# Performance work log

Measured on AMD Instinct MI355X. Metric: run time of the kernel, lower is better.

## Reference

```python
import jax, jax.numpy as jnp
import numpy as np

POOL = 7; SR = 2; SCALE = 1.0 / 16
NUM_CLASSES = 21
NMS_THR = 0.5; MIN_SIZE = 1.0; TOPK = 100; SCORE_THR = 0.05
BBOX_CLIP = float(np.log(1000.0 / 16))


def roi_align(feat, rois):
    # feat: [C,H,W]; rois: [P,4] xyxy in image coords. torchvision aligned=True, sampling_ratio=2.
    C, H, W = feat.shape
    S = POOL * SR
    x0r = rois[:, 0] * SCALE - 0.5
    y0r = rois[:, 1] * SCALE - 0.5
    bw = (rois[:, 2] - rois[:, 0]) * SCALE / POOL
    bh = (rois[:, 3] - rois[:, 1]) * SCALE / POOL
    t = (jnp.arange(S, dtype=feat.dtype) + 0.5) / SR  # sample offsets in bin units
    ys = y0r[:, None] + bh[:, None] * t  # [P,S]
    xs = x0r[:, None] + bw[:, None] * t  # [P,S]
    vy = (ys >= -1.0) & (ys <= H)
    vx = (xs >= -1.0) & (xs <= W)
    y = jnp.clip(ys, 0.0, H - 1)
    x = jnp.clip(xs, 0.0, W - 1)
    yl = jnp.floor(y).astype(jnp.int32); xl = jnp.floor(x).astype(jnp.int32)
    yh = jnp.minimum(yl + 1, H - 1);     xh = jnp.minimum(xl + 1, W - 1)
    ly = y - yl; lx = x - xl
    hy = 1.0 - ly; hx = 1.0 - lx

    def g(Yi, Xi):  # -> [C,P,S,S]
        return feat[:, Yi[:, :, None], Xi[:, None, :]]

    val = (g(yl, xl) * (hy[:, :, None] * hx[:, None, :])
         + g(yl, xh) * (hy[:, :, None] * lx[:, None, :])
         + g(yh, xl) * (ly[:, :, None] * hx[:, None, :])
         + g(yh, xh) * (ly[:, :, None] * lx[:, None, :]))
    val = val * (vy[:, :, None] & vx[:, None, :])[None].astype(feat.dtype)
    P = rois.shape[0]
    val = val.reshape(C, P, POOL, SR, POOL, SR).mean(axis=(3, 5))  # avg over 2x2 samples/bin
    return val.transpose(1, 0, 2, 3)  # [P,C,POOL,POOL]


def decode(pred, proposals):
    # pred: [N,K,4] (dx,dy,dw,dh); proposals: [N,4]
    w = proposals[:, 2] - proposals[:, 0]
    h = proposals[:, 3] - proposals[:, 1]
    cx = proposals[:, 0] + 0.5 * w
    cy = proposals[:, 1] + 0.5 * h
    dx, dy = pred[..., 0], pred[..., 1]
    dw = jnp.minimum(pred[..., 2], BBOX_CLIP)
    dh = jnp.minimum(pred[..., 3], BBOX_CLIP)
    pcx = dx * w[:, None] + cx[:, None]
    pcy = dy * h[:, None] + cy[:, None]
    pw = jnp.exp(dw) * w[:, None]
    ph = jnp.exp(dh) * h[:, None]
    return jnp.stack([pcx - 0.5 * pw, pcy - 0.5 * ph, pcx + 0.5 * pw, pcy + 0.5 * ph], axis=-1)


def box_iou(b):
    x1, y1, x2, y2 = b[:, 0], b[:, 1], b[:, 2], b[:, 3]
    area = (x2 - x1) * (y2 - y1)
    iw = jnp.maximum(jnp.minimum(x2[:, None], x2[None, :]) - jnp.maximum(x1[:, None], x1[None, :]), 0.0)
    ih = jnp.maximum(jnp.minimum(y2[:, None], y2[None, :]) - jnp.maximum(y1[:, None], y1[None, :]), 0.0)
    inter = iw * ih
    return inter / (area[:, None] + area[None, :] - inter)


def filter_predictions(boxes, labels, scores):
    # score threshold + min-size + per-class greedy NMS + topK, static shapes (padded to TOPK)
    N = scores.shape[0]
    ws = boxes[:, 2] - boxes[:, 0]
    hs = boxes[:, 3] - boxes[:, 1]
    valid = (scores > SCORE_THR) & (ws >= MIN_SIZE) & (hs >= MIN_SIZE)
    skey = jnp.where(valid, scores, -jnp.inf)
    order = jnp.argsort(-skey)
    b = boxes[order]; s = skey[order]; l = labels[order]; v = valid[order]
    # batched_nms via per-class coordinate offset
    off = jax.lax.stop_gradient(jnp.max(boxes) + 1.0)
    ob = jax.lax.stop_gradient(b) + (l.astype(b.dtype) * off)[:, None]
    iou = box_iou(ob)  # [N,N]
    idx = jnp.arange(N)

    def body(keep, i):
        sup = (iou[i] > NMS_THR) & keep[i] & (idx > i)
        return keep & ~sup, None

    keep, _ = jax.lax.scan(body, v, idx)
    rank = jnp.cumsum(keep) - 1
    final = keep & (rank < TOPK)
    pick = jnp.argsort(jnp.where(final, idx, N))[:TOPK]  # kept indices in score order, padded
    ok = final[pick]
    out_boxes = jnp.where(ok[:, None], b[pick], 0.0)
    out_scores = jnp.where(ok, s[pick], 0.0)
    out_labels = jnp.where(ok, l[pick], -1)
    return out_boxes, out_labels, out_scores


def roi_head_forward(image, feat, proposals, fc6_w, fc6_b, fc7_w, fc7_b, cls_w, cls_b, reg_w, reg_b):
    H_img, W_img = image.shape[-2], image.shape[-1]
    pooled = roi_align(feat[0], proposals)  # [P,C,7,7]
    x = pooled.reshape(pooled.shape[0], -1)
    x = jax.nn.relu(x @ fc6_w.T + fc6_b)
    x = jax.nn.relu(x @ fc7_w.T + fc7_b)
    cls_scores = x @ cls_w.T + cls_b                       # [P,K]
    box_pred = (x @ reg_w.T + reg_b).reshape(-1, NUM_CLASSES, 4)
    boxes = decode(box_pred, proposals)                    # [P,K,4]
    scores = jax.nn.softmax(cls_scores, axis=-1)
    boxes = jnp.stack([boxes[..., 0].clip(0, W_img), boxes[..., 1].clip(0, H_img),
                       boxes[..., 2].clip(0, W_img), boxes[..., 3].clip(0, H_img)], axis=-1)
    labels = jnp.broadcast_to(jnp.arange(NUM_CLASSES), scores.shape)
    boxes = boxes[:, 1:].reshape(-1, 4)
    scores = scores[:, 1:].reshape(-1)
    labels = (labels[:, 1:] - 1).reshape(-1)
    return filter_predictions(boxes, labels, scores)


def setup_inputs() -> dict:
    key = jax.random.key(0)
    ks = jax.random.split(key, 12)
    H_img, W_img = 800, 1072
    P, C = 300, 512
    image = jnp.zeros((1, 3, H_img, W_img), jnp.float32)
    feat = jax.random.normal(ks[0], (1, C, H_img // 16, W_img // 16), jnp.float32)
    cx = jax.random.uniform(ks[1], (P,)) * W_img
    cy = jax.random.uniform(ks[2], (P,)) * H_img
    bw = 20.0 + jax.random.uniform(ks[3], (P,)) * 300.0
    bh = 20.0 + jax.random.uniform(ks[4], (P,)) * 300.0
    proposals = jnp.stack([jnp.clip(cx - bw / 2, 0, W_img), jnp.clip(cy - bh / 2, 0, H_img),
                           jnp.clip(cx + bw / 2, 0, W_img), jnp.clip(cy + bh / 2, 0, H_img)], axis=1)
    fin = C * POOL * POOL  # 25088
    D = 1024
    fc6_w = jax.random.normal(ks[5], (D, fin), jnp.float32) / np.sqrt(fin)
    fc6_b = jnp.zeros((D,), jnp.float32)
    fc7_w = jax.random.normal(ks[6], (D, D), jnp.float32) / np.sqrt(D)
    fc7_b = jnp.zeros((D,), jnp.float32)
    cls_w = jax.random.normal(ks[7], (NUM_CLASSES, D), jnp.float32) / np.sqrt(D)
    cls_b = jnp.zeros((NUM_CLASSES,), jnp.float32)
    reg_w = jax.random.normal(ks[8], (NUM_CLASSES * 4, D), jnp.float32) * 0.001
    reg_b = jnp.zeros((NUM_CLASSES * 4,), jnp.float32)
    return {"image": image, "feat": feat, "proposals": proposals,
            "fc6_w": fc6_w, "fc6_b": fc6_b, "fc7_w": fc7_w, "fc7_b": fc7_b,
            "cls_w": cls_w, "cls_b": cls_b, "reg_w": reg_w, "reg_b": reg_b}


def reference(image, feat, proposals, fc6_w, fc6_b, fc7_w, fc7_b, cls_w, cls_b, reg_w, reg_b):
    return roi_head_forward(image, feat, proposals, fc6_w, fc6_b, fc7_w, fc7_b, cls_w, cls_b, reg_w, reg_b)
```

## Files before the change

kernel.cpp:

```cpp
#include <hip/hip_runtime.h>
#include <hip/hip_bf16.h>
#include <math.h>

#define P_N   300
#define C_N   512
#define H_F   50
#define W_F   67
#define HW_F  3350
#define D_N   1024
#define FIN   25088
#define NCLS  21
#define NCAND 6000
#define W_IMG 1072.0f
#define H_IMG 800.0f
#define BBOX_CLIP_F 4.135166556742356f
#define KS6   28
#define STEPS6_PER_Z 28
#define KS7   16
#define STEPS7_PER_Z 2
#define KSH   16
#define STEPSH_PER_Z 2
#define NHEAD 128
#define NW    96
#define A_SCALE 16.0f
#define B_SCALE 256.0f
#define O_SCALE (1.0f / 4096.0f)
#define TBLK  1680

typedef __attribute__((ext_vector_type(8)))  _Float16 half8;
typedef __attribute__((ext_vector_type(16))) float    f32x16;

__device__ __forceinline__ void splitA(float f, _Float16& h, _Float16& l) {
  float fs = f * A_SCALE;
  h = (_Float16)fs;
  l = (_Float16)(fs - (float)h);
}

__device__ __forceinline__ int swz(int slot, int ks) {
  return slot ^ ((slot >> 5) & 1) ^ (((slot >> 3) & 1) << 1) ^ ((ks & 1) << 2);
}

__device__ __forceinline__ int blob_half_idx(int row, int j8) {
  const int ksW = j8 >> 1, kc8 = j8 & 1;
  const int mf = row >> 5;
  return (mf * 2 + ksW) * 512 + swz((kc8 << 5) | (row & 31), ksW) * 8;
}

__global__ __launch_bounds__(256) void prep_transpose(const float* __restrict__ feat,
                                                      float* __restrict__ ft,
                                                      const float* __restrict__ cls_w,
                                                      const float* __restrict__ cls_b,
                                                      const float* __restrict__ reg_w,
                                                      const float* __restrict__ reg_b,
                                                      float* __restrict__ Wpad,
                                                      float* __restrict__ bpad,
                                                      int* __restrict__ vcount) {
  __shared__ float tile[32][33];
  const int bid = blockIdx.x;
  const int tid = threadIdx.x;
  if (bid < TBLK) {
    const int bx = bid % 105, byy = bid / 105;
    const int s0 = bx * 32, c0 = byy * 32;
    const int tx = tid & 31, ty = tid >> 5;
    for (int r = ty; r < 32; r += 8) {
      int c = c0 + r, s = s0 + tx;
      tile[r][tx] = (s < HW_F) ? feat[(size_t)c * HW_F + s] : 0.0f;
    }
    __syncthreads();
    for (int r = ty; r < 32; r += 8) {
      int s = s0 + r, c = c0 + tx;
      if (s < HW_F) ft[(size_t)s * C_N + c] = tile[tx][r];
    }
  } else {
    const int row = bid - TBLK;
    if (row == 0 && tid == 0) *vcount = 0;
    const float* src = (row < NCLS) ? (cls_w + (size_t)row * D_N)
                     : (row < 105)  ? (reg_w + (size_t)(row - NCLS) * D_N) : nullptr;
    float4 v = make_float4(0.f, 0.f, 0.f, 0.f);
    if (src) v = reinterpret_cast<const float4*>(src)[tid];
    reinterpret_cast<float4*>(Wpad + (size_t)row * D_N)[tid] = v;
    if (tid == 0)
      bpad[row] = (row < NCLS) ? cls_b[row] : (row < 105) ? reg_b[row - NCLS] : 0.0f;
  }
}

__global__ __launch_bounds__(256, 3) void roi_align_k(const float* __restrict__ ft,
                                                      const float* __restrict__ rois,
                                                      _Float16* __restrict__ Xhi,
                                                      _Float16* __restrict__ Xlo) {
  __shared__ _Float16 hbuf[12544] __attribute__((aligned(16)));
  __shared__ _Float16 lbuf[12544] __attribute__((aligned(16)));
  __shared__ float g_ly[14], g_hy[14], g_lx[14], g_hx[14];
  __shared__ int   g_yoL[14], g_yoH[14], g_xoL[14], g_xoH[14];

  const int p   = blockIdx.x;
  const int ch  = blockIdx.y;
  const int tid = threadIdx.x;

  if (tid < 14) {
    const float rx0 = rois[p*4+0], ry0 = rois[p*4+1], rx1 = rois[p*4+2], ry1 = rois[p*4+3];
    const float x0r = rx0 * 0.0625f - 0.5f;
    const float y0r = ry0 * 0.0625f - 0.5f;
    const float bw  = (rx1 - rx0) * 0.0625f * (1.0f / 7.0f);
    const float bh  = (ry1 - ry0) * 0.0625f * (1.0f / 7.0f);
    const float t   = ((float)tid + 0.5f) * 0.5f;

    const float ys = y0r + bh * t;
    const bool vy = (ys >= -1.0f) && (ys <= (float)H_F);
    float y = fminf(fmaxf(ys, 0.0f), (float)(H_F - 1));
    int yi = (int)floorf(y);
    const int yh = min(yi + 1, H_F - 1);
    float ly = y - (float)yi, hy = 1.0f - (y - (float)yi);
    if (!vy) { ly = 0.0f; hy = 0.0f; }
    g_ly[tid] = ly; g_hy[tid] = hy;
    g_yoL[tid] = yi * (W_F * C_N); g_yoH[tid] = yh * (W_F * C_N);

    const float xs = x0r + bw * t;
    const bool vx = (xs >= -1.0f) && (xs <= (float)W_F);
    float x = fminf(fmaxf(xs, 0.0f), (float)(W_F - 1));
    int xi = (int)floorf(x);
    const int xh = min(xi + 1, W_F - 1);
    float lx = x - (float)xi, hx = 1.0f - (x - (float)xi);
    if (!vx) { lx = 0.0f; hx = 0.0f; }
    g_lx[tid] = lx; g_hx[tid] = hx;
    g_xoL[tid] = xi * C_N; g_xoH[tid] = xh * C_N;
  }
  __syncthreads();

  const float* ftc = ft + ch * 256 + tid;
#pragma unroll 4
  for (int cell = 0; cell < 49; ++cell) {
    const int py = cell / 7;
    const int px = cell - py * 7;
    float acc = 0.0f;
#pragma unroll
    for (int sy = 0; sy < 2; ++sy) {
      const int iy = 2 * py + sy;
      const float ly = g_ly[iy], hy = g_hy[iy];
      const int yoL = g_yoL[iy], yoH = g_yoH[iy];
#pragma unroll
      for (int sx = 0; sx < 2; ++sx) {
        const int ix = 2 * px + sx;
        const float lx = g_lx[ix], hx = g_hx[ix];
        const int xoL = g_xoL[ix], xoH = g_xoH[ix];
        acc += (hy*hx)*ftc[yoL+xoL] + (hy*lx)*ftc[yoL+xoH]
             + (ly*hx)*ftc[yoH+xoL] + (ly*lx)*ftc[yoH+xoH];
      }
    }
    _Float16 h, l;
    splitA(acc * 0.25f, h, l);
    hbuf[tid * 49 + cell] = h;
    lbuf[tid * 49 + cell] = l;
  }
  __syncthreads();

  const size_t base = (size_t)p * FIN + (size_t)ch * 12544;
  const uint4* hs = (const uint4*)hbuf;
  const uint4* ls = (const uint4*)lbuf;
  uint4* dh = (uint4*)(Xhi + base);
  uint4* dl = (uint4*)(Xlo + base);
  for (int k = tid; k < 1568; k += 256) { dh[k] = hs[k]; dl[k] = ls[k]; }
}

__global__ __launch_bounds__(256) void reshuffle_x(const _Float16* __restrict__ Shi,
                                                   const _Float16* __restrict__ Slo,
                                                   char* __restrict__ blob,
                                                   int M2, int K) {
  __shared__ _Float16 buf[8192] __attribute__((aligned(16)));
  const int tile = blockIdx.x, step = blockIdx.y;
  const int tid = threadIdx.x;
  const int steps = K >> 5;
#pragma unroll
  for (int i = 0; i < 4; ++i) {
    const int g = tid + i * 256;
    const int half = g >> 9;
    const int row = (g >> 2) & 127;
    const int j8 = g & 3;
    const int gm = tile * 128 + row;
    uint4 v = make_uint4(0, 0, 0, 0);
    if (gm < M2) {
      const _Float16* src = (half ? Slo : Shi) + (size_t)gm * K + (step << 5) + (j8 << 3);
      v = *reinterpret_cast<const uint4*>(src);
    }
    *reinterpret_cast<uint4*>(buf + half * 4096 + blob_half_idx(row, j8)) = v;
  }
  __syncthreads();
  uint4* dst = (uint4*)(blob + (((size_t)tile * steps + step) << 14));
  const uint4* s = (const uint4*)buf;
#pragma unroll
  for (int i = 0; i < 4; ++i) dst[tid + i * 256] = s[tid + i * 256];
}

__global__ __launch_bounds__(256, 3) void gemm_f16_3p(
    const char* __restrict__ Ablob, const float* __restrict__ Wt, float* __restrict__ Pt,
    int M, int K, int steps_per_z, int ldc)
{
  __shared__ _Float16 lds[16384] __attribute__((aligned(16)));
  const int tid  = threadIdx.x;
  const int lane = tid & 63, wave = tid >> 6;
  const int wm = wave >> 1, wn = wave & 1;

  const int GX = gridDim.x, GY = gridDim.y;
  const int T  = GX * GY * gridDim.z;
  int flat = blockIdx.x + GX * (blockIdx.y + GY * blockIdx.z);
  if ((T & 7) == 0) flat = (flat & 7) * (T >> 3) + (flat >> 3);
  const int bx = flat % GX;
  const int by = (flat / GX) % GY;
  const int bz = flat / (GX * GY);

  const int m0 = bx * 128, n0 = by * 128;
  const int steps_total = K >> 5;
  const int s0 = bz * steps_per_z;
  const int s1 = min(s0 + steps_per_z, steps_total);

  f32x16 acc[2][2];
#pragma unroll
  for (int a = 0; a < 2; ++a)
#pragma unroll
    for (int b = 0; b < 2; ++b)
#pragma unroll
      for (int r = 0; r < 16; ++r) acc[a][b][r] = 0.f;

  const int srow = tid >> 2;
  const int j8   = tid & 3;
  const int ksW  = j8 >> 1, kc8 = j8 & 1;
  const int wslot = swz((kc8 << 5) | (srow & 31), ksW);

  for (int step = s0; step < s1; ++step) {
    const int kb = step << 5;
    const char* Ab = Ablob + (((size_t)bx * steps_total + step) << 14);
#pragma unroll
    for (int c2 = 0; c2 < 4; ++c2) {
      const int off = ((wave << 2) + c2) << 10;
      __builtin_amdgcn_global_load_lds(
          (const __attribute__((address_space(1))) uint32_t*)(Ab + off + (lane << 4)),
          (__attribute__((address_space(3))) uint32_t*)((char*)lds + off),
          16, 0, 0);
    }
#pragma unroll
    for (int half = 0; half < 2; ++half) {
      const int n = srow + half * 64;
      const float* wp = Wt + (size_t)(n0 + n) * K + kb + j8 * 8;
      const float4 f0 = *reinterpret_cast<const float4*>(wp);
      const float4 f1 = *reinterpret_cast<const float4*>(wp + 4);
      float fv[8] = {f0.x, f0.y, f0.z, f0.w, f1.x, f1.y, f1.z, f1.w};
      union { _Float16 h[8]; uint4 v; } uh, ul;
#pragma unroll
      for (int e = 0; e < 8; ++e) {
        float fs = fv[e] * B_SCALE;
        uh.h[e] = (_Float16)fs;
        ul.h[e] = (_Float16)(fs - (float)uh.h[e]);
      }
      const int nf = n >> 5;
      const int base = 8192 + (nf * 2 + ksW) * 512 + wslot * 8;
      *reinterpret_cast<uint4*>(&lds[base])        = uh.v;
      *reinterpret_cast<uint4*>(&lds[4096 + base]) = ul.v;
    }
    __syncthreads();
#pragma unroll
    for (int ks = 0; ks < 2; ++ks) {
      const int rslot = swz(lane, ks) * 8;
      half8 ah[2], al[2], bh[2], bl[2];
#pragma unroll
      for (int mi = 0; mi < 2; ++mi) {
        const int mf = wm * 2 + mi;
        ah[mi] = *reinterpret_cast<const half8*>(&lds[(mf * 2 + ks) * 512 + rslot]);
        al[mi] = *reinterpret_cast<const half8*>(&lds[4096 + (mf * 2 + ks) * 512 + rslot]);
      }
#pragma unroll
      for (int ni = 0; ni < 2; ++ni) {
        const int nf = wn * 2 + ni;
        bh[ni] = *reinterpret_cast<const half8*>(&lds[8192  + (nf * 2 + ks) * 512 + rslot]);
        bl[ni] = *reinterpret_cast<const half8*>(&lds[12288 + (nf * 2 + ks) * 512 + rslot]);
      }
#pragma unroll
      for (int mi = 0; mi < 2; ++mi)
#pragma unroll
        for (int ni = 0; ni < 2; ++ni) {
          acc[mi][ni] = __builtin_amdgcn_mfma_f32_32x32x16_f16(ah[mi], bh[ni], acc[mi][ni], 0, 0, 0);
          acc[mi][ni] = __builtin_amdgcn_mfma_f32_32x32x16_f16(ah[mi], bl[ni], acc[mi][ni], 0, 0, 0);
          acc[mi][ni] = __builtin_amdgcn_mfma_f32_32x32x16_f16(al[mi], bh[ni], acc[mi][ni], 0, 0, 0);
        }
    }
    __syncthreads();
  }
  const int col = lane & 31, rhi = lane >> 5;
  float* outp = Pt + (size_t)bz * ((size_t)M * ldc);
#pragma unroll
  for (int mi = 0; mi < 2; ++mi)
#pragma unroll
    for (int ni = 0; ni < 2; ++ni) {
      const int n = n0 + (wn * 2 + ni) * 32 + col;
      if (n >= ldc) continue;
#pragma unroll
      for (int r = 0; r < 16; ++r) {
        const int m = m0 + (wm * 2 + mi) * 32 + ((r & 3) + 8 * (r >> 2) + 4 * rhi);
        if (m < M) outp[(size_t)m * ldc + n] = acc[mi][ni][r] * O_SCALE;
      }
    }
}

__global__ __launch_bounds__(256) void reduce_frag(const float* __restrict__ Pt,
                                                   const float* __restrict__ bias,
                                                   char* __restrict__ blob,
                                                   int KS, int stepsB) {
  const int g = blockIdx.x * 256 + threadIdx.x;
  if (g >= P_N * 128) return;
  const int m = g >> 7;
  const int gg = g & 127;
  const int n0 = gg << 3;
  float s[8];
#pragma unroll
  for (int e = 0; e < 8; ++e) s[e] = bias[n0 + e];
  for (int k2 = 0; k2 < KS; ++k2) {
    const float* pp = Pt + ((size_t)k2 * P_N + m) * D_N + n0;
    const float4 a = *reinterpret_cast<const float4*>(pp);
    const float4 b = *reinterpret_cast<const float4*>(pp + 4);
    s[0]+=a.x; s[1]+=a.y; s[2]+=a.z; s[3]+=a.w;
    s[4]+=b.x; s[5]+=b.y; s[6]+=b.z; s[7]+=b.w;
  }
  union { _Float16 h[8]; uint4 v; } uh, ul;
#pragma unroll
  for (int e = 0; e < 8; ++e) {
    float r = fmaxf(s[e], 0.0f);
    _Float16 h, l; splitA(r, h, l);
    uh.h[e] = h; ul.h[e] = l;
  }
  const int tile = m >> 7, row = m & 127;
  const int step = gg >> 2, j8 = gg & 3;
  _Float16* dst = (_Float16*)(blob + (((size_t)tile * stepsB + step) << 14));
  const int hidx = blob_half_idx(row, j8);
  *reinterpret_cast<uint4*>(dst + hidx) = uh.v;
  *reinterpret_cast<uint4*>(dst + 4096 + hidx) = ul.v;
}

__global__ __launch_bounds__(256) void reduce_bias(const float* __restrict__ Pt,
                                                   const float* __restrict__ bias,
                                                   float* __restrict__ out_f32,
                                                   int MN, int KS, int nmask) {
  int i = blockIdx.x * 256 + threadIdx.x;
  if (i >= MN) return;
  float s = 0.0f;
  for (int k = 0; k < KS; ++k) s += Pt[(size_t)k * MN + i];
  s += bias[i & nmask];
  out_f32[i] = s;
}

__global__ __launch_bounds__(64) void decode_kernel(const float* __restrict__ logits,
                                                    const float* __restrict__ props,
                                                    float* __restrict__ cboxes,
                                                    unsigned long long* __restrict__ ckeys,
                                                    int* __restrict__ vcount) {
  const int p = blockIdx.x;
  const int lane = threadIdx.x;
  const float* lg = logits + (size_t)p * NHEAD;

  float s = (lane < NCLS) ? lg[lane] : -__builtin_inff();
  float mx = s;
#pragma unroll
  for (int off = 32; off > 0; off >>= 1) mx = fmaxf(mx, __shfl_xor(mx, off));
  float e = (lane < NCLS) ? expf(s - mx) : 0.0f;
  float sum = e;
#pragma unroll
  for (int off = 32; off > 0; off >>= 1) sum += __shfl_xor(sum, off);
  const float sm = e / sum;

  if (lane >= 1 && lane < NCLS) {
    const int c = lane;
    const float x0 = props[p*4+0], y0 = props[p*4+1], x1 = props[p*4+2], y1 = props[p*4+3];
    const float w = x1 - x0, hh = y1 - y0;
    const float cx = x0 + 0.5f * w, cy = y0 + 0.5f * hh;
    const float dx = lg[NCLS + c*4 + 0];
    const float dy = lg[NCLS + c*4 + 1];
    const float dw = fminf(lg[NCLS + c*4 + 2], BBOX_CLIP_F);
    const float dh = fminf(lg[NCLS + c*4 + 3], BBOX_CLIP_F);
    const float pcx = dx * w + cx, pcy = dy * hh + cy;
    const float pw = expf(dw) * w, ph = expf(dh) * hh;
    float bx0 = pcx - 0.5f * pw, by0 = pcy - 0.5f * ph;
    float bx1 = pcx + 0.5f * pw, by1 = pcy + 0.5f * ph;
    bx0 = fminf(fmaxf(bx0, 0.0f), W_IMG);
    by0 = fminf(fmaxf(by0, 0.0f), H_IMG);
    bx1 = fminf(fmaxf(bx1, 0.0f), W_IMG);
    by1 = fminf(fmaxf(by1, 0.0f), H_IMG);
    const int idx = p * 20 + (c - 1);
    cboxes[idx*4+0] = bx0; cboxes[idx*4+1] = by0;
    cboxes[idx*4+2] = bx1; cboxes[idx*4+3] = by1;
    const bool valid = (sm > 0.05f) && ((bx1 - bx0) >= 1.0f) && ((by1 - by0) >= 1.0f);
    if (valid) {
      int pos = atomicAdd(vcount, 1);
      unsigned u = __float_as_uint(sm);
      ckeys[pos] = ((unsigned long long)(~u) << 32) | (unsigned)idx;
    }
  }
}

__global__ __launch_bounds__(1024) void sort_gather(const unsigned long long* __restrict__ ckeys,
                                                    const int* __restrict__ vcount,
                                                    const float* __restrict__ cboxes,
                                                    float4* __restrict__ sbox,
                                                    float* __restrict__ sscore,
                                                    int* __restrict__ slab) {
  __shared__ unsigned long long keys[8192];
  const int tid = threadIdx.x;
  const int V = *vcount;
  int Npad = 64; while (Npad < V) Npad <<= 1;
  for (int i = tid; i < Npad; i += 1024)
    keys[i] = (i < V) ? ckeys[i] : ~0ULL;
  __syncthreads();
  for (int kk = 2; kk <= Npad; kk <<= 1) {
    for (int j = kk >> 1; j > 0; j >>= 1) {
      for (int i = tid; i < Npad; i += 1024) {
        int ij = i ^ j;
        if (ij > i) {
          unsigned long long a = keys[i], b = keys[ij];
          bool up = ((i & kk) == 0);
          if ((a > b) == up) { keys[i] = b; keys[ij] = a; }
        }
      }
      __syncthreads();
    }
  }
  for (int i = tid; i < V; i += 1024) {
    unsigned long long key = keys[i];
    int idx = (int)(key & 0xffffffffu);
    sbox[i]   = *reinterpret_cast<const float4*>(&cboxes[(size_t)idx * 4]);
    sscore[i] = __uint_as_float(~(unsigned)(key >> 32));
    slab[i]   = idx % 20;
  }
}

__global__ __launch_bounds__(256) void iou_matrix(const float4* __restrict__ sbox,
                                                  const int* __restrict__ slab,
                                                  const int* __restrict__ vcount,
                                                  unsigned long long* __restrict__ mask) {
  const int V = *vcount;
  const int i = blockIdx.x * 4 + (threadIdx.x >> 6);
  const int lane = threadIdx.x & 63;
  if (i >= V) return;
  const float4 bi = sbox[i];
  const int li = slab[i];
  const float ai = (bi.z - bi.x) * (bi.w - bi.y);
  const int nw = (V + 63) >> 6;
  for (int w = 0; w < nw; ++w) {
    const int j = (w << 6) + lane;
    bool sup = false;
    if (j > i && j < V && slab[j] == li) {
      const float4 bj = sbox[j];
      const float iw = fminf(bi.z, bj.z) - fmaxf(bi.x, bj.x);
      const float ih = fminf(bi.w, bj.w) - fmaxf(bi.y, bj.y);
      const float inter = fmaxf(iw, 0.0f) * fmaxf(ih, 0.0f);
      const float aj = (bj.z - bj.x) * (bj.w - bj.y);
      sup = inter / (ai + aj - inter) > 0.5f;
    }
    const unsigned long long m = __ballot(sup);
    if (lane == 0) mask[(size_t)i * NW + w] = m;
  }
}

__device__ __forceinline__ unsigned long long bcast_live(unsigned long long live0,
                                                         unsigned long long live1, int w) {
  union { unsigned long long u; uint2 v; } t;
  t.u = (w < 64) ? live0 : live1;
  const int src = w & 63;
  const unsigned lo = __shfl(t.v.x, src);
  const unsigned hi = __shfl(t.v.y, src);
  return ((unsigned long long)hi << 32) | lo;
}

__global__ __launch_bounds__(64) void nms_scan(const float4* __restrict__ sbox,
                                               const float* __restrict__ sscore,
                                               const int* __restrict__ slab,
                                               const int* __restrict__ vcount,
                                               const unsigned long long* __restrict__ mask,
                                               float* __restrict__ out) {
  const int lane = threadIdx.x;
  const int V = min(*vcount, NCAND);
  const int nw = (V + 63) >> 6;
  unsigned long long live0 = ~0ULL, live1 = ~0ULL;
  int nk = 0;
  for (int w = 0; w < nw && nk < 100; ++w) {
    const int nb = V - (w << 6);
    const unsigned long long vmask = (nb >= 64) ? ~0ULL : ((1ULL << nb) - 1ULL);
    unsigned long long wv = bcast_live(live0, live1, w) & vmask;
    while (wv && nk < 100) {
      const int b = __ffsll((long long)wv) - 1;
      const int i = (w << 6) + b;
      if (lane == 0) {
        const float4 bb = sbox[i];
        out[nk*4+0] = bb.x; out[nk*4+1] = bb.y; out[nk*4+2] = bb.z; out[nk*4+3] = bb.w;
        out[400 + nk] = (float)slab[i];
        out[500 + nk] = sscore[i];
      }
      const unsigned long long* mrow = mask + (size_t)i * NW;
      if (lane < nw) live0 &= ~mrow[lane];
      if (64 + lane < nw) live1 &= ~mrow[64 + lane];
      nk++;
      wv = bcast_live(live0, live1, w) & vmask;
      wv &= (b == 63) ? 0ULL : ~((2ULL << b) - 1ULL);
    }
  }
  for (int r = nk + lane; r < 100; r += 64) {
    out[r*4+0] = 0.0f; out[r*4+1] = 0.0f; out[r*4+2] = 0.0f; out[r*4+3] = 0.0f;
    out[400 + r] = -1.0f;
    out[500 + r] = 0.0f;
  }
}

extern "C" void kernel_launch(void* const* d_in, const int* in_sizes, int n_in,
                              void* d_out, int out_size, void* d_ws, size_t ws_size,
                              hipStream_t stream) {
  const float* feat   = (const float*)d_in[1];
  const float* props  = (const float*)d_in[2];
  const float* fc6_w  = (const float*)d_in[3];
  const float* fc6_b  = (const float*)d_in[4];
  const float* fc7_w  = (const float*)d_in[5];
  const float* fc7_b  = (const float*)d_in[6];
  const float* cls_w  = (const float*)d_in[7];
  const float* cls_b  = (const float*)d_in[8];
  const float* reg_w  = (const float*)d_in[9];
  const float* reg_b  = (const float*)d_in[10];

  char* ws = (char*)d_ws;
  const size_t XSZ = (size_t)P_N * FIN * 2;
  const size_t R1  = (size_t)KS6 * P_N * D_N * 4;
  _Float16* Xhi = (_Float16*)ws;
  _Float16* Xlo = (_Float16*)(ws + XSZ);
  float*    Pt  = (float*)ws;
  char* reg2 = ws + R1;
  float* ft   = (float*)reg2;
  char*  Xb   = reg2;
  const size_t XBSZ = (size_t)3 * 784 * 16384;
  size_t off = R1 + XBSZ;
  auto alloc = [&](size_t bytes) -> void* {
    void* p = ws + off;
    off += (bytes + 255) & ~(size_t)255;
    return p;
  };
  char*  h6b   = (char*)alloc((size_t)3 * 32 * 16384);
  char*  h7b   = (char*)alloc((size_t)3 * 32 * 16384);
  float* Wpad  = (float*)alloc((size_t)NHEAD * D_N * 4);
  float* bpad  = (float*)alloc((size_t)NHEAD * 4);
  float* logits= (float*)alloc((size_t)P_N * NHEAD * 4);
  float* cboxes= (float*)alloc((size_t)NCAND * 4 * 4);
  unsigned long long* ckeys = (unsigned long long*)alloc((size_t)NCAND * 8);
  float4* sbox = (float4*)alloc((size_t)NCAND * 16);
  float* sscore= (float*)alloc((size_t)NCAND * 4);
  int*   slab  = (int*)alloc((size_t)NCAND * 4);
  unsigned long long* supmask = (unsigned long long*)alloc((size_t)NCAND * NW * 8);
  int*   vcount= (int*)alloc(256);
  (void)ws_size; (void)in_sizes; (void)n_in; (void)out_size;

  prep_transpose<<<TBLK + NHEAD, 256, 0, stream>>>(feat, ft, cls_w, cls_b, reg_w, reg_b,
                                                   Wpad, bpad, vcount);
  roi_align_k<<<dim3(P_N, 2), 256, 0, stream>>>(ft, props, Xhi, Xlo);
  reshuffle_x<<<dim3(3, 784), 256, 0, stream>>>(Xhi, Xlo, Xb, P_N, FIN);
  gemm_f16_3p<<<dim3(3, 8, KS6), 256, 0, stream>>>(Xb, fc6_w, Pt, P_N, FIN, STEPS6_PER_Z, D_N);
  reduce_frag<<<150, 256, 0, stream>>>(Pt, fc6_b, h6b, KS6, 32);
  gemm_f16_3p<<<dim3(3, 8, KS7), 256, 0, stream>>>(h6b, fc7_w, Pt, P_N, D_N, STEPS7_PER_Z, D_N);
  reduce_frag<<<150, 256, 0, stream>>>(Pt, fc7_b, h7b, KS7, 32);
  gemm_f16_3p<<<dim3(3, 1, KSH), 256, 0, stream>>>(h7b, Wpad, Pt, P_N, D_N, STEPSH_PER_Z, NHEAD);
  reduce_bias<<<(P_N * NHEAD + 255) / 256, 256, 0, stream>>>(
      Pt, bpad, logits, P_N * NHEAD, KSH, NHEAD - 1);
  decode_kernel<<<P_N, 64, 0, stream>>>(logits, props, cboxes, ckeys, vcount);
  sort_gather<<<1, 1024, 0, stream>>>(ckeys, vcount, cboxes, sbox, sscore, slab);
  iou_matrix<<<(NCAND + 3) / 4, 256, 0, stream>>>(sbox, slab, vcount, supmask);
  nms_scan<<<1, 64, 0, stream>>>(sbox, sscore, slab, vcount, supmask, (float*)d_out);
}
```

Before: 339.3 us.

## Double-buffer LDS in split-K GEMM and widen block to 512 threads

```diff
diff --git a/kernel.cpp b/kernel.cpp
--- a/kernel.cpp
+++ b/kernel.cpp
@@ -191,14 +191,14 @@
   for (int i = 0; i < 4; ++i) dst[tid + i * 256] = s[tid + i * 256];
 }
 
-__global__ __launch_bounds__(256, 3) void gemm_f16_3p(
+__global__ __launch_bounds__(512, 4) void gemm_f16_3p(
     const char* __restrict__ Ablob, const float* __restrict__ Wt, float* __restrict__ Pt,
     int M, int K, int steps_per_z, int ldc)
 {
-  __shared__ _Float16 lds[16384] __attribute__((aligned(16)));
+  __shared__ _Float16 lds[32768] __attribute__((aligned(16)));
   const int tid  = threadIdx.x;
   const int lane = tid & 63, wave = tid >> 6;
-  const int wm = wave >> 1, wn = wave & 1;
+  const int wm = wave >> 2, wn = wave & 3;
 
   const int GX = gridDim.x, GY = gridDim.y;
   const int T  = GX * GY * gridDim.z;
@@ -213,91 +213,92 @@
   const int s0 = bz * steps_per_z;
   const int s1 = min(s0 + steps_per_z, steps_total);
 
-  f32x16 acc[2][2];
+  f32x16 acc[2];
 #pragma unroll
   for (int a = 0; a < 2; ++a)
 #pragma unroll
-    for (int b = 0; b < 2; ++b)
-#pragma unroll
-      for (int r = 0; r < 16; ++r) acc[a][b][r] = 0.f;
+    for (int r = 0; r < 16; ++r) acc[a][r] = 0.f;
 
   const int srow = tid >> 2;
   const int j8   = tid & 3;
   const int ksW  = j8 >> 1, kc8 = j8 & 1;
   const int wslot = swz((kc8 << 5) | (srow & 31), ksW);
-
-  for (int step = s0; step < s1; ++step) {
+  const int nfB  = srow >> 5;
+
+  auto stage = [&](int buf, int step) {
     const int kb = step << 5;
+    char* ldsb = (char*)lds + (buf << 15);
     const char* Ab = Ablob + (((size_t)bx * steps_total + step) << 14);
 #pragma unroll
-    for (int c2 = 0; c2 < 4; ++c2) {
-      const int off = ((wave << 2) + c2) << 10;
+    for (int c2 = 0; c2 < 2; ++c2) {
+      const int off = ((wave * 2 + c2) << 10);
       __builtin_amdgcn_global_load_lds(
           (const __attribute__((address_space(1))) uint32_t*)(Ab + off + (lane << 4)),
-          (__attribute__((address_space(3))) uint32_t*)((char*)lds + off),
+          (__attribute__((address_space(3))) uint32_t*)(ldsb + off),
           16, 0, 0);
     }
-#pragma unroll
-    for (int half = 0; half < 2; ++half) {
-      const int n = srow + half * 64;
-      const float* wp = Wt + (size_t)(n0 + n) * K + kb + j8 * 8;
-      const float4 f0 = *reinterpret_cast<const float4*>(wp);
-      const float4 f1 = *reinterpret_cast<const float4*>(wp + 4);
-      float fv[8] = {f0.x, f0.y, f0.z, f0.w, f1.x, f1.y, f1.z, f1.w};
-      union { _Float16 h[8]; uint4 v; } uh, ul;
-#pragma unroll
-      for (int e = 0; e < 8; ++e) {
-        float fs = fv[e] * B_SCALE;
-        uh.h[e] = (_Float16)fs;
-        ul.h[e] = (_Float16)(fs - (float)uh.h[e]);
-      }
-      const int nf = n >> 5;
-      const int base = 8192 + (nf * 2 + ksW) * 512 + wslot * 8;
-      *reinterpret_cast<uint4*>(&lds[base])        = uh.v;
-      *reinterpret_cast<uint4*>(&lds[4096 + base]) = ul.v;
-    }
-    __syncthreads();
+    const float* wp = Wt + (size_t)(n0 + srow) * K + kb + j8 * 8;
+    const float4 f0 = *reinterpret_cast<const float4*>(wp);
+    const float4 f1 = *reinterpret_cast<const float4*>(wp + 4);
+    float fv[8] = {f0.x, f0.y, f0.z, f0.w, f1.x, f1.y, f1.z, f1.w};
+    union { _Float16 h[8]; uint4 v; } uh, ul;
+#pragma unroll
+    for (int e = 0; e < 8; ++e) {
+      float fs = fv[e] * B_SCALE;
+      uh.h[e] = (_Float16)fs;
+      ul.h[e] = (_Float16)(fs - (float)uh.h[e]);
+    }
+    _Float16* ldsh = (_Float16*)ldsb;
+    const int base = 8192 + (nfB * 2 + ksW) * 512 + wslot * 8;
+    *reinterpret_cast<uint4*>(&ldsh[base])        = uh.v;
+    *reinterpret_cast<uint4*>(&ldsh[4096 + base]) = ul.v;
+  };
+
+  auto compute = [&](int buf) {
+    _Float16* ldsh = (_Float16*)((char*)lds + (buf << 15));
 #pragma unroll
     for (int ks = 0; ks < 2; ++ks) {
       const int rslot = swz(lane, ks) * 8;
-      half8 ah[2], al[2], bh[2], bl[2];
+      half8 ah[2], al[2], bh, bl;
 #pragma unroll
       for (int mi = 0; mi < 2; ++mi) {
         const int mf = wm * 2 + mi;
-        ah[mi] = *reinterpret_cast<const half8*>(&lds[(mf * 2 + ks) * 512 + rslot]);
-        al[mi] = *reinterpret_cast<const half8*>(&lds[4096 + (mf * 2 + ks) * 512 + rslot]);
+        ah[mi] = *reinterpret_cast<const half8*>(&ldsh[(mf * 2 + ks) * 512 + rslot]);
+        al[mi] = *reinterpret_cast<const half8*>(&ldsh[4096 + (mf * 2 + ks) * 512 + rslot]);
       }
-#pragma unroll
-      for (int ni = 0; ni < 2; ++ni) {
-        const int nf = wn * 2 + ni;
-        bh[ni] = *reinterpret_cast<const half8*>(&lds[8192  + (nf * 2 + ks) * 512 + rslot]);
-        bl[ni] = *reinterpret_cast<const half8*>(&lds[12288 + (nf * 2 + ks) * 512 + rslot]);
+      bh = *reinterpret_cast<const half8*>(&ldsh[8192  + (wn * 2 + ks) * 512 + rslot]);
+      bl = *reinterpret_cast<const half8*>(&ldsh[12288 + (wn * 2 + ks) * 512 + rslot]);
+#pragma unroll
+      for (int mi = 0; mi < 2; ++mi) {
+        acc[mi] = __builtin_amdgcn_mfma_f32_32x32x16_f16(ah[mi], bh, acc[mi], 0, 0, 0);
+        acc[mi] = __builtin_amdgcn_mfma_f32_32x32x16_f16(ah[mi], bl, acc[mi], 0, 0, 0);
+        acc[mi] = __builtin_amdgcn_mfma_f32_32x32x16_f16(al[mi], bh, acc[mi], 0, 0, 0);
       }
-#pragma unroll
-      for (int mi = 0; mi < 2; ++mi)
-#pragma unroll
-        for (int ni = 0; ni < 2; ++ni) {
-          acc[mi][ni] = __builtin_amdgcn_mfma_f32_32x32x16_f16(ah[mi], bh[ni], acc[mi][ni], 0, 0, 0);
-          acc[mi][ni] = __builtin_amdgcn_mfma_f32_32x32x16_f16(ah[mi], bl[ni], acc[mi][ni], 0, 0, 0);
-          acc[mi][ni] = __builtin_amdgcn_mfma_f32_32x32x16_f16(al[mi], bh[ni], acc[mi][ni], 0, 0, 0);
-        }
-    }
+    }
+  };
+
+  if (s0 < s1) stage(0, s0);
+  __syncthreads();
+  int cur = 0;
+  for (int s = s0; s < s1; ++s) {
+    if (s + 1 < s1) stage(cur ^ 1, s + 1);
+    compute(cur);
     __syncthreads();
-  }
+    cur ^= 1;
+  }
+
   const int col = lane & 31, rhi = lane >> 5;
   float* outp = Pt + (size_t)bz * ((size_t)M * ldc);
-#pragma unroll
-  for (int mi = 0; mi < 2; ++mi)
-#pragma unroll
-    for (int ni = 0; ni < 2; ++ni) {
-      const int n = n0 + (wn * 2 + ni) * 32 + col;
-      if (n >= ldc) continue;
+  const int n = n0 + wn * 32 + col;
+  if (n < ldc) {
+#pragma unroll
+    for (int mi = 0; mi < 2; ++mi)
 #pragma unroll
       for (int r = 0; r < 16; ++r) {
         const int m = m0 + (wm * 2 + mi) * 32 + ((r & 3) + 8 * (r >> 2) + 4 * rhi);
-        if (m < M) outp[(size_t)m * ldc + n] = acc[mi][ni][r] * O_SCALE;
+        if (m < M) outp[(size_t)m * ldc + n] = acc[mi][r] * O_SCALE;
       }
-    }
+  }
 }
 
 __global__ __launch_bounds__(256) void reduce_frag(const float* __restrict__ Pt,
@@ -554,11 +555,11 @@
                                                    Wpad, bpad, vcount);
   roi_align_k<<<dim3(P_N, 2), 256, 0, stream>>>(ft, props, Xhi, Xlo);
   reshuffle_x<<<dim3(3, 784), 256, 0, stream>>>(Xhi, Xlo, Xb, P_N, FIN);
-  gemm_f16_3p<<<dim3(3, 8, KS6), 256, 0, stream>>>(Xb, fc6_w, Pt, P_N, FIN, STEPS6_PER_Z, D_N);
+  gemm_f16_3p<<<dim3(3, 8, KS6), 512, 0, stream>>>(Xb, fc6_w, Pt, P_N, FIN, STEPS6_PER_Z, D_N);
   reduce_frag<<<150, 256, 0, stream>>>(Pt, fc6_b, h6b, KS6, 32);
-  gemm_f16_3p<<<dim3(3, 8, KS7), 256, 0, stream>>>(h6b, fc7_w, Pt, P_N, D_N, STEPS7_PER_Z, D_N);
+  gemm_f16_3p<<<dim3(3, 8, KS7), 512, 0, stream>>>(h6b, fc7_w, Pt, P_N, D_N, STEPS7_PER_Z, D_N);
   reduce_frag<<<150, 256, 0, stream>>>(Pt, fc7_b, h7b, KS7, 32);
-  gemm_f16_3p<<<dim3(3, 1, KSH), 256, 0, stream>>>(h7b, Wpad, Pt, P_N, D_N, STEPSH_PER_Z, NHEAD);
+  gemm_f16_3p<<<dim3(3, 1, KSH), 512, 0, stream>>>(h7b, Wpad, Pt, P_N, D_N, STEPSH_PER_Z, NHEAD);
   reduce_bias<<<(P_N * NHEAD + 255) / 256, 256, 0, stream>>>(
       Pt, bpad, logits, P_N * NHEAD, KSH, NHEAD - 1);
   decode_kernel<<<P_N, 64, 0, stream>>>(logits, props, cboxes, ckeys, vcount);
```

Result: slower. 352.1 us (+3.8%).

## Double-buffer GEMM LDS tiles and fuse head split-K reduction into decode

Applied to the files above, without the earlier changes.

```diff
diff --git a/kernel.cpp b/kernel.cpp
--- a/kernel.cpp
+++ b/kernel.cpp
@@ -191,11 +191,11 @@
   for (int i = 0; i < 4; ++i) dst[tid + i * 256] = s[tid + i * 256];
 }
 
-__global__ __launch_bounds__(256, 3) void gemm_f16_3p(
+__global__ __launch_bounds__(256, 2) void gemm_f16_3p(
     const char* __restrict__ Ablob, const float* __restrict__ Wt, float* __restrict__ Pt,
     int M, int K, int steps_per_z, int ldc)
 {
-  __shared__ _Float16 lds[16384] __attribute__((aligned(16)));
+  __shared__ _Float16 lds[32768] __attribute__((aligned(16)));
   const int tid  = threadIdx.x;
   const int lane = tid & 63, wave = tid >> 6;
   const int wm = wave >> 1, wn = wave & 1;
@@ -225,65 +225,101 @@
   const int j8   = tid & 3;
   const int ksW  = j8 >> 1, kc8 = j8 & 1;
   const int wslot = swz((kc8 << 5) | (srow & 31), ksW);
-
-  for (int step = s0; step < s1; ++step) {
-    const int kb = step << 5;
+  const int nf0 = srow >> 5;
+  const int nf1 = (srow + 64) >> 5;
+
+  auto issueA = [&](int buf, int step) {
     const char* Ab = Ablob + (((size_t)bx * steps_total + step) << 14);
+    char* ldsb = (char*)lds + (buf << 15);
 #pragma unroll
     for (int c2 = 0; c2 < 4; ++c2) {
       const int off = ((wave << 2) + c2) << 10;
       __builtin_amdgcn_global_load_lds(
           (const __attribute__((address_space(1))) uint32_t*)(Ab + off + (lane << 4)),
-          (__attribute__((address_space(3))) uint32_t*)((char*)lds + off),
+          (__attribute__((address_space(3))) uint32_t*)(ldsb + off),
           16, 0, 0);
     }
-#pragma unroll
-    for (int half = 0; half < 2; ++half) {
-      const int n = srow + half * 64;
-      const float* wp = Wt + (size_t)(n0 + n) * K + kb + j8 * 8;
-      const float4 f0 = *reinterpret_cast<const float4*>(wp);
-      const float4 f1 = *reinterpret_cast<const float4*>(wp + 4);
-      float fv[8] = {f0.x, f0.y, f0.z, f0.w, f1.x, f1.y, f1.z, f1.w};
-      union { _Float16 h[8]; uint4 v; } uh, ul;
-#pragma unroll
-      for (int e = 0; e < 8; ++e) {
-        float fs = fv[e] * B_SCALE;
-        uh.h[e] = (_Float16)fs;
-        ul.h[e] = (_Float16)(fs - (float)uh.h[e]);
-      }
-      const int nf = n >> 5;
-      const int base = 8192 + (nf * 2 + ksW) * 512 + wslot * 8;
-      *reinterpret_cast<uint4*>(&lds[base])        = uh.v;
-      *reinterpret_cast<uint4*>(&lds[4096 + base]) = ul.v;
-    }
-    __syncthreads();
+  };
+  auto loadB = [&](int step, float4& g0, float4& g1, float4& g2, float4& g3) {
+    const int kb = step << 5;
+    const float* wp0 = Wt + (size_t)(n0 + srow) * K + kb + j8 * 8;
+    const float* wp1 = Wt + (size_t)(n0 + srow + 64) * K + kb + j8 * 8;
+    g0 = *reinterpret_cast<const float4*>(wp0);
+    g1 = *reinterpret_cast<const float4*>(wp0 + 4);
+    g2 = *reinterpret_cast<const float4*>(wp1);
+    g3 = *reinterpret_cast<const float4*>(wp1 + 4);
+  };
+  auto writeB = [&](int buf, float4 g0, float4 g1, float4 g2, float4 g3) {
+    _Float16* ldsh = (_Float16*)((char*)lds + (buf << 15));
+    float fv0[8] = {g0.x, g0.y, g0.z, g0.w, g1.x, g1.y, g1.z, g1.w};
+    float fv1[8] = {g2.x, g2.y, g2.z, g2.w, g3.x, g3.y, g3.z, g3.w};
+    union { _Float16 h[8]; uint4 v; } uh0, ul0, uh1, ul1;
+#pragma unroll
+    for (int e = 0; e < 8; ++e) {
+      float fs0 = fv0[e] * B_SCALE;
+      uh0.h[e] = (_Float16)fs0;
+      ul0.h[e] = (_Float16)(fs0 - (float)uh0.h[e]);
+      float fs1 = fv1[e] * B_SCALE;
+      uh1.h[e] = (_Float16)fs1;
+      ul1.h[e] = (_Float16)(fs1 - (float)uh1.h[e]);
+    }
+    const int base0 = 8192 + (nf0 * 2 + ksW) * 512 + wslot * 8;
+    const int base1 = 8192 + (nf1 * 2 + ksW) * 512 + wslot * 8;
+    *reinterpret_cast<uint4*>(&ldsh[base0])        = uh0.v;
+    *reinterpret_cast<uint4*>(&ldsh[4096 + base0]) = ul0.v;
+    *reinterpret_cast<uint4*>(&ldsh[base1])        = uh1.v;
+    *reinterpret_cast<uint4*>(&ldsh[4096 + base1]) = ul1.v;
+  };
+
+  if (s0 < s1) {
+    issueA(0, s0);
+    float4 g0, g1, g2, g3;
+    loadB(s0, g0, g1, g2, g3);
+    writeB(0, g0, g1, g2, g3);
+  }
+  __syncthreads();
+
+  int cur = 0;
+  for (int s = s0; s < s1; ++s) {
+    _Float16* ldsh = (_Float16*)((char*)lds + (cur << 15));
+    half8 ah[2][2], al[2][2], bh[2][2], bl[2][2];
 #pragma unroll
     for (int ks = 0; ks < 2; ++ks) {
       const int rslot = swz(lane, ks) * 8;
-      half8 ah[2], al[2], bh[2], bl[2];
 #pragma unroll
       for (int mi = 0; mi < 2; ++mi) {
         const int mf = wm * 2 + mi;
-        ah[mi] = *reinterpret_cast<const half8*>(&lds[(mf * 2 + ks) * 512 + rslot]);
-        al[mi] = *reinterpret_cast<const half8*>(&lds[4096 + (mf * 2 + ks) * 512 + rslot]);
+        ah[ks][mi] = *reinterpret_cast<const half8*>(&ldsh[(mf * 2 + ks) * 512 + rslot]);
+        al[ks][mi] = *reinterpret_cast<const half8*>(&ldsh[4096 + (mf * 2 + ks) * 512 + rslot]);
       }
 #pragma unroll
       for (int ni = 0; ni < 2; ++ni) {
         const int nf = wn * 2 + ni;
-        bh[ni] = *reinterpret_cast<const half8*>(&lds[8192  + (nf * 2 + ks) * 512 + rslot]);
-        bl[ni] = *reinterpret_cast<const half8*>(&lds[12288 + (nf * 2 + ks) * 512 + rslot]);
+        bh[ks][ni] = *reinterpret_cast<const half8*>(&ldsh[8192  + (nf * 2 + ks) * 512 + rslot]);
+        bl[ks][ni] = *reinterpret_cast<const half8*>(&ldsh[12288 + (nf * 2 + ks) * 512 + rslot]);
       }
+    }
+    const bool hasNext = (s + 1 < s1);
+    float4 g0, g1, g2, g3;
+    if (hasNext) {
+      issueA(cur ^ 1, s + 1);
+      loadB(s + 1, g0, g1, g2, g3);
+    }
+#pragma unroll
+    for (int ks = 0; ks < 2; ++ks)
 #pragma unroll
       for (int mi = 0; mi < 2; ++mi)
 #pragma unroll
         for (int ni = 0; ni < 2; ++ni) {
-          acc[mi][ni] = __builtin_amdgcn_mfma_f32_32x32x16_f16(ah[mi], bh[ni], acc[mi][ni], 0, 0, 0);
-          acc[mi][ni] = __builtin_amdgcn_mfma_f32_32x32x16_f16(ah[mi], bl[ni], acc[mi][ni], 0, 0, 0);
-          acc[mi][ni] = __builtin_amdgcn_mfma_f32_32x32x16_f16(al[mi], bh[ni], acc[mi][ni], 0, 0, 0);
+          acc[mi][ni] = __builtin_amdgcn_mfma_f32_32x32x16_f16(ah[ks][mi], bh[ks][ni], acc[mi][ni], 0, 0, 0);
+          acc[mi][ni] = __builtin_amdgcn_mfma_f32_32x32x16_f16(ah[ks][mi], bl[ks][ni], acc[mi][ni], 0, 0, 0);
+          acc[mi][ni] = __builtin_amdgcn_mfma_f32_32x32x16_f16(al[ks][mi], bh[ks][ni], acc[mi][ni], 0, 0, 0);
         }
-    }
+    if (hasNext) writeB(cur ^ 1, g0, g1, g2, g3);
     __syncthreads();
-  }
+    cur ^= 1;
+  }
+
   const int col = lane & 31, rhi = lane >> 5;
   float* outp = Pt + (size_t)bz * ((size_t)M * ldc);
 #pragma unroll
@@ -334,26 +370,23 @@
   *reinterpret_cast<uint4*>(dst + 4096 + hidx) = ul.v;
 }
 
-__global__ __launch_bounds__(256) void reduce_bias(const float* __restrict__ Pt,
-                                                   const float* __restrict__ bias,
-                                                   float* __restrict__ out_f32,
-                                                   int MN, int KS, int nmask) {
-  int i = blockIdx.x * 256 + threadIdx.x;
-  if (i >= MN) return;
-  float s = 0.0f;
-  for (int k = 0; k < KS; ++k) s += Pt[(size_t)k * MN + i];
-  s += bias[i & nmask];
-  out_f32[i] = s;
-}
-
-__global__ __launch_bounds__(64) void decode_kernel(const float* __restrict__ logits,
+__global__ __launch_bounds__(64) void decode_kernel(const float* __restrict__ Pt,
+                                                    const float* __restrict__ bpad,
                                                     const float* __restrict__ props,
                                                     float* __restrict__ cboxes,
                                                     unsigned long long* __restrict__ ckeys,
                                                     int* __restrict__ vcount) {
   const int p = blockIdx.x;
   const int lane = threadIdx.x;
-  const float* lg = logits + (size_t)p * NHEAD;
+  __shared__ float lg[NHEAD];
+
+  for (int o = lane; o < NHEAD; o += 64) {
+    float s = 0.0f;
+    for (int k = 0; k < KSH; ++k)
+      s += Pt[((size_t)k * P_N + p) * NHEAD + o];
+    lg[o] = s + bpad[o];
+  }
+  __syncthreads();
 
   float s = (lane < NCLS) ? lg[lane] : -__builtin_inff();
   float mx = s;
@@ -540,7 +573,6 @@
   char*  h7b   = (char*)alloc((size_t)3 * 32 * 16384);
   float* Wpad  = (float*)alloc((size_t)NHEAD * D_N * 4);
   float* bpad  = (float*)alloc((size_t)NHEAD * 4);
-  float* logits= (float*)alloc((size_t)P_N * NHEAD * 4);
   float* cboxes= (float*)alloc((size_t)NCAND * 4 * 4);
   unsigned long long* ckeys = (unsigned long long*)alloc((size_t)NCAND * 8);
   float4* sbox = (float4*)alloc((size_t)NCAND * 16);
@@ -559,9 +591,7 @@
   gemm_f16_3p<<<dim3(3, 8, KS7), 256, 0, stream>>>(h6b, fc7_w, Pt, P_N, D_N, STEPS7_PER_Z, D_N);
   reduce_frag<<<150, 256, 0, stream>>>(Pt, fc7_b, h7b, KS7, 32);
   gemm_f16_3p<<<dim3(3, 1, KSH), 256, 0, stream>>>(h7b, Wpad, Pt, P_N, D_N, STEPSH_PER_Z, NHEAD);
-  reduce_bias<<<(P_N * NHEAD + 255) / 256, 256, 0, stream>>>(
-      Pt, bpad, logits, P_N * NHEAD, KSH, NHEAD - 1);
-  decode_kernel<<<P_N, 64, 0, stream>>>(logits, props, cboxes, ckeys, vcount);
+  decode_kernel<<<P_N, 64, 0, stream>>>(Pt, bpad, props, cboxes, ckeys, vcount);
   sort_gather<<<1, 1024, 0, stream>>>(ckeys, vcount, cboxes, sbox, sscore, slab);
   iou_matrix<<<(NCAND + 3) / 4, 256, 0, stream>>>(sbox, slab, vcount, supmask);
   nms_scan<<<1, 64, 0, stream>>>(sbox, sscore, slab, vcount, supmask, (float*)d_out);
```

New measurement: 345.1 us. Within noise of the previous version (+1.7%).

## Process two K-steps per GEMM barrier and fuse head reduction into decode

Applied to the files above, without the earlier changes.

```diff
diff --git a/kernel.cpp b/kernel.cpp
--- a/kernel.cpp
+++ b/kernel.cpp
@@ -191,11 +191,11 @@
   for (int i = 0; i < 4; ++i) dst[tid + i * 256] = s[tid + i * 256];
 }
 
-__global__ __launch_bounds__(256, 3) void gemm_f16_3p(
+__global__ __launch_bounds__(256) void gemm_f16_3p(
     const char* __restrict__ Ablob, const float* __restrict__ Wt, float* __restrict__ Pt,
     int M, int K, int steps_per_z, int ldc)
 {
-  __shared__ _Float16 lds[16384] __attribute__((aligned(16)));
+  __shared__ _Float16 lds[32768] __attribute__((aligned(16)));
   const int tid  = threadIdx.x;
   const int lane = tid & 63, wave = tid >> 6;
   const int wm = wave >> 1, wn = wave & 1;
@@ -225,62 +225,72 @@
   const int j8   = tid & 3;
   const int ksW  = j8 >> 1, kc8 = j8 & 1;
   const int wslot = swz((kc8 << 5) | (srow & 31), ksW);
-
-  for (int step = s0; step < s1; ++step) {
-    const int kb = step << 5;
-    const char* Ab = Ablob + (((size_t)bx * steps_total + step) << 14);
-#pragma unroll
-    for (int c2 = 0; c2 < 4; ++c2) {
-      const int off = ((wave << 2) + c2) << 10;
+  const int nf0 = srow >> 5;
+  const int nf1 = (srow + 64) >> 5;
+
+  for (int s = s0; s < s1; s += 2) {
+    const char* Ab = Ablob + (((size_t)bx * steps_total + s) << 14);
+#pragma unroll
+    for (int c2 = 0; c2 < 8; ++c2) {
+      const int off = ((wave << 3) + c2) << 10;
       __builtin_amdgcn_global_load_lds(
           (const __attribute__((address_space(1))) uint32_t*)(Ab + off + (lane << 4)),
           (__attribute__((address_space(3))) uint32_t*)((char*)lds + off),
           16, 0, 0);
     }
 #pragma unroll
-    for (int half = 0; half < 2; ++half) {
-      const int n = srow + half * 64;
-      const float* wp = Wt + (size_t)(n0 + n) * K + kb + j8 * 8;
-      const float4 f0 = *reinterpret_cast<const float4*>(wp);
-      const float4 f1 = *reinterpret_cast<const float4*>(wp + 4);
-      float fv[8] = {f0.x, f0.y, f0.z, f0.w, f1.x, f1.y, f1.z, f1.w};
-      union { _Float16 h[8]; uint4 v; } uh, ul;
-#pragma unroll
-      for (int e = 0; e < 8; ++e) {
-        float fs = fv[e] * B_SCALE;
-        uh.h[e] = (_Float16)fs;
-        ul.h[e] = (_Float16)(fs - (float)uh.h[e]);
+    for (int sub = 0; sub < 2; ++sub) {
+      const int kb = (s + sub) << 5;
+#pragma unroll
+      for (int half = 0; half < 2; ++half) {
+        const int n = srow + half * 64;
+        const float* wp = Wt + (size_t)(n0 + n) * K + kb + j8 * 8;
+        const float4 f0 = *reinterpret_cast<const float4*>(wp);
+        const float4 f1 = *reinterpret_cast<const float4*>(wp + 4);
+        float fv[8] = {f0.x, f0.y, f0.z, f0.w, f1.x, f1.y, f1.z, f1.w};
+        union { _Float16 h[8]; uint4 v; } uh, ul;
+#pragma unroll
+        for (int e = 0; e < 8; ++e) {
+          float fs = fv[e] * B_SCALE;
+          uh.h[e] = (_Float16)fs;
+          ul.h[e] = (_Float16)(fs - (float)uh.h[e]);
+        }
+        const int nf = half ? nf1 : nf0;
+        const int base = 16384 + sub * 8192 + (nf * 2 + ksW) * 512 + wslot * 8;
+        *reinterpret_cast<uint4*>(&lds[base])        = uh.v;
+        *reinterpret_cast<uint4*>(&lds[4096 + base]) = ul.v;
       }
-      const int nf = n >> 5;
-      const int base = 8192 + (nf * 2 + ksW) * 512 + wslot * 8;
-      *reinterpret_cast<uint4*>(&lds[base])        = uh.v;
-      *reinterpret_cast<uint4*>(&lds[4096 + base]) = ul.v;
     }
     __syncthreads();
 #pragma unroll
-    for (int ks = 0; ks < 2; ++ks) {
-      const int rslot = swz(lane, ks) * 8;
-      half8 ah[2], al[2], bh[2], bl[2];
-#pragma unroll
-      for (int mi = 0; mi < 2; ++mi) {
-        const int mf = wm * 2 + mi;
-        ah[mi] = *reinterpret_cast<const half8*>(&lds[(mf * 2 + ks) * 512 + rslot]);
-        al[mi] = *reinterpret_cast<const half8*>(&lds[4096 + (mf * 2 + ks) * 512 + rslot]);
+    for (int sub = 0; sub < 2; ++sub) {
+      _Float16* ldsA = lds + sub * 8192;
+      _Float16* ldsB = lds + 16384 + sub * 8192;
+#pragma unroll
+      for (int ks = 0; ks < 2; ++ks) {
+        const int rslot = swz(lane, ks) * 8;
+        half8 ah[2], al[2], bh[2], bl[2];
+#pragma unroll
+        for (int mi = 0; mi < 2; ++mi) {
+          const int mf = wm * 2 + mi;
+          ah[mi] = *reinterpret_cast<const half8*>(&ldsA[(mf * 2 + ks) * 512 + rslot]);
+          al[mi] = *reinterpret_cast<const half8*>(&ldsA[4096 + (mf * 2 + ks) * 512 + rslot]);
+        }
+#pragma unroll
+        for (int ni = 0; ni < 2; ++ni) {
+          const int nf = wn * 2 + ni;
+          bh[ni] = *reinterpret_cast<const half8*>(&ldsB[(nf * 2 + ks) * 512 + rslot]);
+          bl[ni] = *reinterpret_cast<const half8*>(&ldsB[4096 + (nf * 2 + ks) * 512 + rslot]);
+        }
+#pragma unroll
+        for (int mi = 0; mi < 2; ++mi)
+#pragma unroll
+          for (int ni = 0; ni < 2; ++ni) {
+            acc[mi][ni] = __builtin_amdgcn_mfma_f32_32x32x16_f16(ah[mi], bh[ni], acc[mi][ni], 0, 0, 0);
+            acc[mi][ni] = __builtin_amdgcn_mfma_f32_32x32x16_f16(ah[mi], bl[ni], acc[mi][ni], 0, 0, 0);
+            acc[mi][ni] = __builtin_amdgcn_mfma_f32_32x32x16_f16(al[mi], bh[ni], acc[mi][ni], 0, 0, 0);
+          }
       }
-#pragma unroll
-      for (int ni = 0; ni < 2; ++ni) {
-        const int nf = wn * 2 + ni;
-        bh[ni] = *reinterpret_cast<const half8*>(&lds[8192  + (nf * 2 + ks) * 512 + rslot]);
-        bl[ni] = *reinterpret_cast<const half8*>(&lds[12288 + (nf * 2 + ks) * 512 + rslot]);
-      }
-#pragma unroll
-      for (int mi = 0; mi < 2; ++mi)
-#pragma unroll
-        for (int ni = 0; ni < 2; ++ni) {
-          acc[mi][ni] = __builtin_amdgcn_mfma_f32_32x32x16_f16(ah[mi], bh[ni], acc[mi][ni], 0, 0, 0);
-          acc[mi][ni] = __builtin_amdgcn_mfma_f32_32x32x16_f16(ah[mi], bl[ni], acc[mi][ni], 0, 0, 0);
-          acc[mi][ni] = __builtin_amdgcn_mfma_f32_32x32x16_f16(al[mi], bh[ni], acc[mi][ni], 0, 0, 0);
-        }
     }
     __syncthreads();
   }
@@ -334,26 +344,23 @@
   *reinterpret_cast<uint4*>(dst + 4096 + hidx) = ul.v;
 }
 
-__global__ __launch_bounds__(256) void reduce_bias(const float* __restrict__ Pt,
-                                                   const float* __restrict__ bias,
-                                                   float* __restrict__ out_f32,
-                                                   int MN, int KS, int nmask) {
-  int i = blockIdx.x * 256 + threadIdx.x;
-  if (i >= MN) return;
-  float s = 0.0f;
-  for (int k = 0; k < KS; ++k) s += Pt[(size_t)k * MN + i];
-  s += bias[i & nmask];
-  out_f32[i] = s;
-}
-
-__global__ __launch_bounds__(64) void decode_kernel(const float* __restrict__ logits,
+__global__ __launch_bounds__(64) void decode_kernel(const float* __restrict__ Pt,
+                                                    const float* __restrict__ bpad,
                                                     const float* __restrict__ props,
                                                     float* __restrict__ cboxes,
                                                     unsigned long long* __restrict__ ckeys,
                                                     int* __restrict__ vcount) {
   const int p = blockIdx.x;
   const int lane = threadIdx.x;
-  const float* lg = logits + (size_t)p * NHEAD;
+  __shared__ float lg[NHEAD];
+
+  for (int o = lane; o < NHEAD; o += 64) {
+    float s = 0.0f;
+    for (int k = 0; k < KSH; ++k)
+      s += Pt[((size_t)k * P_N + p) * NHEAD + o];
+    lg[o] = s + bpad[o];
+  }
+  __syncthreads();
 
   float s = (lane < NCLS) ? lg[lane] : -__builtin_inff();
   float mx = s;
@@ -540,7 +547,6 @@
   char*  h7b   = (char*)alloc((size_t)3 * 32 * 16384);
   float* Wpad  = (float*)alloc((size_t)NHEAD * D_N * 4);
   float* bpad  = (float*)alloc((size_t)NHEAD * 4);
-  float* logits= (float*)alloc((size_t)P_N * NHEAD * 4);
   float* cboxes= (float*)alloc((size_t)NCAND * 4 * 4);
   unsigned long long* ckeys = (unsigned long long*)alloc((size_t)NCAND * 8);
   float4* sbox = (float4*)alloc((size_t)NCAND * 16);
@@ -559,9 +565,7 @@
   gemm_f16_3p<<<dim3(3, 8, KS7), 256, 0, stream>>>(h6b, fc7_w, Pt, P_N, D_N, STEPS7_PER_Z, D_N);
   reduce_frag<<<150, 256, 0, stream>>>(Pt, fc7_b, h7b, KS7, 32);
   gemm_f16_3p<<<dim3(3, 1, KSH), 256, 0, stream>>>(h7b, Wpad, Pt, P_N, D_N, STEPSH_PER_Z, NHEAD);
-  reduce_bias<<<(P_N * NHEAD + 255) / 256, 256, 0, stream>>>(
-      Pt, bpad, logits, P_N * NHEAD, KSH, NHEAD - 1);
-  decode_kernel<<<P_N, 64, 0, stream>>>(logits, props, cboxes, ckeys, vcount);
+  decode_kernel<<<P_N, 64, 0, stream>>>(Pt, bpad, props, cboxes, ckeys, vcount);
   sort_gather<<<1, 1024, 0, stream>>>(ckeys, vcount, cboxes, sbox, sscore, slab);
   iou_matrix<<<(NCAND + 3) / 4, 256, 0, stream>>>(sbox, slab, vcount, supmask);
   nms_scan<<<1, 64, 0, stream>>>(sbox, sscore, slab, vcount, supmask, (float*)d_out);
```

New measurement: 355.6 us. +4.8%, slower.
